# Optimization experiments

Hardware: AMD Instinct MI355X
Metric: run time of the kernel (lower is better)

Reference implementation:

```python
import jax, jax.numpy as jnp
import numpy as np

N_NODES = 50000
N_EDGES = 800000
D_IN = 128
D_OUT = 128
BN_EPS = 1e-5


def setup_inputs() -> dict:
    key = jax.random.key(0)
    ks = jax.random.split(key, 6)
    feat = jax.random.normal(ks[0], (N_NODES, D_IN), dtype=jnp.float32)
    src = jax.random.randint(ks[1], (N_EDGES,), 0, N_NODES, dtype=jnp.int32)
    dst = jax.random.randint(ks[2], (N_EDGES,), 0, N_NODES, dtype=jnp.int32)
    W = jax.random.normal(ks[3], (D_IN, D_OUT), dtype=jnp.float32) * (1.0 / np.sqrt(D_IN))
    b = jnp.zeros((D_OUT,), dtype=jnp.float32)
    a1 = jnp.full((1,), 0.25, dtype=jnp.float32)  # PReLU inside GraphConv
    gamma = jnp.ones((D_OUT,), dtype=jnp.float32)
    beta = jnp.zeros((D_OUT,), dtype=jnp.float32)
    a2 = jnp.full((1,), 0.25, dtype=jnp.float32)  # PReLU after BN
    return {"feat": feat, "src": src, "dst": dst, "W": W, "b": b,
            "a1": a1, "gamma": gamma, "beta": beta, "a2": a2}


def _prelu(x, a):
    return jnp.where(x >= 0, x, a * x)


def reference(feat, src, dst, W, b, a1, gamma, beta, a2):
    # Degrees (DGL clamps to min 1 to avoid inf norms)
    ones_e = jnp.ones((src.shape[0],), dtype=feat.dtype)
    out_deg = jnp.clip(jax.ops.segment_sum(ones_e, src, num_segments=N_NODES), 1.0)
    in_deg = jnp.clip(jax.ops.segment_sum(ones_e, dst, num_segments=N_NODES), 1.0)
    norm_src = jax.lax.rsqrt(out_deg)[:, None]   # [N,1]
    norm_dst = jax.lax.rsqrt(in_deg)[:, None]    # [N,1]

    # Dropout (eval mode -> identity), source normalization, projection
    h = (feat * norm_src) @ W                    # [N, D_OUT]
    # Gather-scatter neighbor aggregation (SpMM): sum over incoming edges
    msg = h[src]                                 # [E, D_OUT]
    agg = jax.ops.segment_sum(msg, dst, num_segments=N_NODES)  # [N, D_OUT]
    h = agg * norm_dst + b                       # dst normalization + bias
    h = _prelu(h, a1)                            # GraphConv activation

    # BatchNorm1d over node dimension (training-mode batch stats, biased var)
    mean = jnp.mean(h, axis=0)
    var = jnp.mean((h - mean) ** 2, axis=0)
    h = (h - mean) * jax.lax.rsqrt(var + BN_EPS) * gamma + beta

    return _prelu(h, a2)
```

## Files before the change

kernel.cpp:

```cpp
#include <hip/hip_runtime.h>
#include <hip/hip_bf16.h>

#define N_NODES 50000
#define N_EDGES 800000
#define D 128
#define BN_EPS 1e-5f
#define ELLW 64
#define PROJ_LDK 136
#define SPMM_BLOCKS 1564

#define BINS 128
#define BIN_RANGE 391
#define BINCAP 8192
#define A_EPT 13
#define A_BLOCKS 256

typedef __attribute__((ext_vector_type(8))) short bf16x8;
typedef __attribute__((ext_vector_type(4))) float f32x4;

__device__ inline float bf_lo(unsigned u) { union { unsigned x; float f; } c; c.x = u << 16; return c.f; }
__device__ inline float bf_hi(unsigned u) { union { unsigned x; float f; } c; c.x = u & 0xffff0000u; return c.f; }
__device__ inline unsigned short f2bf(float f) {
    union { float f; unsigned u; } c; c.f = f;
    unsigned u = c.u;
    u += 0x7fff + ((u >> 16) & 1);
    return (unsigned short)(u >> 16);
}
__device__ inline unsigned pack2bf(float a, float b) {
    return (unsigned)f2bf(a) | ((unsigned)f2bf(b) << 16);
}

__global__ __launch_bounds__(256) void bucket_kernel(const int* __restrict__ src,
                                                     const int* __restrict__ dst,
                                                     int* __restrict__ gdbase,
                                                     int* __restrict__ gsbase,
                                                     unsigned* __restrict__ dbkt,
                                                     unsigned short* __restrict__ sbkt) {
    __shared__ int dcnt[BINS], scnt[BINS], dbase[BINS], sbase[BINS];
    const int tid = threadIdx.x;
    if (tid < BINS) { dcnt[tid] = 0; scnt[tid] = 0; }
    __syncthreads();

    const int e0 = blockIdx.x * (256 * A_EPT) + tid;
    int s[A_EPT], t[A_EPT], dr[A_EPT], sr[A_EPT];
    #pragma unroll
    for (int k = 0; k < A_EPT; ++k) {
        int e = e0 + k * 256;
        if (e < N_EDGES) { s[k] = src[e]; t[k] = dst[e]; }
        else             { s[k] = -1;     t[k] = -1;     }
    }
    #pragma unroll
    for (int k = 0; k < A_EPT; ++k) {
        if (t[k] >= 0) dr[k] = atomicAdd(&dcnt[t[k] / BIN_RANGE], 1);
        if (s[k] >= 0) sr[k] = atomicAdd(&scnt[s[k] / BIN_RANGE], 1);
    }
    __syncthreads();
    if (tid < BINS) {
        dbase[tid] = atomicAdd(&gdbase[tid], dcnt[tid]);
        sbase[tid] = atomicAdd(&gsbase[tid], scnt[tid]);
    }
    __syncthreads();
    #pragma unroll
    for (int k = 0; k < A_EPT; ++k) {
        if (t[k] >= 0) {
            int b = t[k] / BIN_RANGE;
            int p = dbase[b] + dr[k];
            if (p < BINCAP)
                dbkt[b * BINCAP + p] = (unsigned)s[k] | ((unsigned)(t[k] - b * BIN_RANGE) << 16);
        }
        if (s[k] >= 0) {
            int b = s[k] / BIN_RANGE;
            int p = sbase[b] + sr[k];
            if (p < BINCAP)
                sbkt[b * BINCAP + p] = (unsigned short)(s[k] - b * BIN_RANGE);
        }
    }
}

__global__ __launch_bounds__(1024) void build_kernel(const int* __restrict__ gdbase,
                                                     const int* __restrict__ gsbase,
                                                     const unsigned* __restrict__ dbkt,
                                                     const unsigned short* __restrict__ sbkt,
                                                     unsigned short* __restrict__ ell,
                                                     int* __restrict__ cnt,
                                                     int* __restrict__ deg_out) {
    __shared__ int hist[BIN_RANGE];
    const int tid = threadIdx.x;
    const int bin = blockIdx.x & (BINS - 1);
    const int lo  = bin * BIN_RANGE;

    for (int i = tid; i < BIN_RANGE; i += 1024) hist[i] = 0;
    __syncthreads();

    if (blockIdx.x < BINS) {
        int count = gdbase[bin]; if (count > BINCAP) count = BINCAP;
        const unsigned* bkt = dbkt + bin * BINCAP;
        int i = tid;
        for (; i + 3072 < count; i += 4096) {
            unsigned e0 = bkt[i], e1 = bkt[i + 1024], e2 = bkt[i + 2048], e3 = bkt[i + 3072];
            int r0 = atomicAdd(&hist[e0 >> 16], 1);
            int r1 = atomicAdd(&hist[e1 >> 16], 1);
            int r2 = atomicAdd(&hist[e2 >> 16], 1);
            int r3 = atomicAdd(&hist[e3 >> 16], 1);
            if (r0 < ELLW) ell[(size_t)(lo + (e0 >> 16)) * ELLW + r0] = (unsigned short)(e0 & 0xffffu);
            if (r1 < ELLW) ell[(size_t)(lo + (e1 >> 16)) * ELLW + r1] = (unsigned short)(e1 & 0xffffu);
            if (r2 < ELLW) ell[(size_t)(lo + (e2 >> 16)) * ELLW + r2] = (unsigned short)(e2 & 0xffffu);
            if (r3 < ELLW) ell[(size_t)(lo + (e3 >> 16)) * ELLW + r3] = (unsigned short)(e3 & 0xffffu);
        }
        for (; i < count; i += 1024) {
            unsigned e = bkt[i];
            int r = atomicAdd(&hist[e >> 16], 1);
            if (r < ELLW) ell[(size_t)(lo + (e >> 16)) * ELLW + r] = (unsigned short)(e & 0xffffu);
        }
        __syncthreads();
        for (int j = tid; j < BIN_RANGE; j += 1024)
            if (lo + j < N_NODES) cnt[lo + j] = hist[j];
    } else {
        int count = gsbase[bin]; if (count > BINCAP) count = BINCAP;
        const unsigned short* bkt = sbkt + bin * BINCAP;
        int i = tid;
        for (; i + 3072 < count; i += 4096) {
            int v0 = bkt[i], v1 = bkt[i + 1024], v2 = bkt[i + 2048], v3 = bkt[i + 3072];
            atomicAdd(&hist[v0], 1); atomicAdd(&hist[v1], 1);
            atomicAdd(&hist[v2], 1); atomicAdd(&hist[v3], 1);
        }
        for (; i < count; i += 1024) atomicAdd(&hist[bkt[i]], 1);
        __syncthreads();
        for (int j = tid; j < BIN_RANGE; j += 1024)
            if (lo + j < N_NODES) deg_out[lo + j] = hist[j];
    }
}

__global__ __launch_bounds__(256, 2) void proj_kernel(const float* __restrict__ feat,
                                                      const float* __restrict__ W,
                                                      const int* __restrict__ deg_out,
                                                      unsigned short* __restrict__ h) {
    __shared__ unsigned short Wt[D * PROJ_LDK];
    __shared__ unsigned short As[64 * PROJ_LDK];
    __shared__ float nrmS[64];

    const int tid  = threadIdx.x;
    const int wave = tid >> 6;
    const int lane = tid & 63;
    const int quad = lane >> 4;
    const int l16  = lane & 15;

    for (int idx = tid; idx < D * D; idx += 256) {
        int k = idx >> 7, d = idx & 127;
        Wt[d * PROJ_LDK + k] = f2bf(W[idx]);
    }
    __syncthreads();

    bf16x8 breg[8][4];
    #pragma unroll
    for (int dt = 0; dt < 8; ++dt)
        #pragma unroll
        for (int kk = 0; kk < 4; ++kk)
            breg[dt][kk] = *(const bf16x8*)&Wt[(dt * 16 + l16) * PROJ_LDK + kk * 32 + quad * 8];

    const int n_tiles = (N_NODES + 63) / 64;
    for (int tile = blockIdx.x; tile < n_tiles; tile += gridDim.x) {
        const int base = tile * 64;
        __syncthreads();
        if (tid < 64) {
            int n = base + tid;
            int dg = (n < N_NODES) ? deg_out[n] : 1;
            nrmS[tid] = rsqrtf((float)(dg < 1 ? 1 : dg));
        }
        __syncthreads();
        for (int idx = tid; idx < 64 * 32; idx += 256) {
            int r = idx >> 5, c4 = idx & 31;
            int n = base + r;
            float4 v = (n < N_NODES) ? ((const float4*)(feat + (size_t)n * D))[c4]
                                     : make_float4(0.f, 0.f, 0.f, 0.f);
            float nm = nrmS[r];
            unsigned short* pp = &As[r * PROJ_LDK + c4 * 4];
            pp[0] = f2bf(v.x * nm); pp[1] = f2bf(v.y * nm);
            pp[2] = f2bf(v.z * nm); pp[3] = f2bf(v.w * nm);
        }
        __syncthreads();

        f32x4 acc[8];
        #pragma unroll
        for (int dt = 0; dt < 8; ++dt) acc[dt] = (f32x4){0.f, 0.f, 0.f, 0.f};

        #pragma unroll
        for (int kk = 0; kk < 4; ++kk) {
            bf16x8 af = *(const bf16x8*)&As[(wave * 16 + l16) * PROJ_LDK + kk * 32 + quad * 8];
            #pragma unroll
            for (int dt = 0; dt < 8; ++dt)
                acc[dt] = __builtin_amdgcn_mfma_f32_16x16x32_bf16(af, breg[dt][kk], acc[dt], 0, 0, 0);
        }

        #pragma unroll
        for (int dt = 0; dt < 8; ++dt) {
            #pragma unroll
            for (int r = 0; r < 4; ++r) {
                int n = base + wave * 16 + quad * 4 + r;
                if (n < N_NODES)
                    h[(size_t)n * D + dt * 16 + l16] = f2bf(acc[dt][r]);
            }
        }
    }
}

#define ACCA(v) { accA[0] += bf_lo((v).x); accA[1] += bf_hi((v).x); \
                  accA[2] += bf_lo((v).y); accA[3] += bf_hi((v).y); \
                  accA[4] += bf_lo((v).z); accA[5] += bf_hi((v).z); \
                  accA[6] += bf_lo((v).w); accA[7] += bf_hi((v).w); }
#define ACCB(v) { accB[0] += bf_lo((v).x); accB[1] += bf_hi((v).x); \
                  accB[2] += bf_lo((v).y); accB[3] += bf_hi((v).y); \
                  accB[4] += bf_lo((v).z); accB[5] += bf_hi((v).z); \
                  accB[6] += bf_lo((v).w); accB[7] += bf_hi((v).w); }
#define GA(sid) { uint4 vv = *(const uint4*)(h + (size_t)(sid) * D + coff); ACCA(vv); }
#define GB(sid) { uint4 vv = *(const uint4*)(h + (size_t)(sid) * D + coff); ACCB(vv); }

__global__ __launch_bounds__(256) void spmm_kernel(const int* __restrict__ cnt,
                                                   const unsigned short* __restrict__ ell,
                                                   const unsigned short* __restrict__ h,
                                                   const float* __restrict__ b,
                                                   const float* __restrict__ a1,
                                                   unsigned short* __restrict__ h2,
                                                   float* __restrict__ bn_sum,
                                                   float* __restrict__ bn_sumsq) {
    const int tid  = threadIdx.x;
    const int l16  = tid & 15;
    const int slot = (blockIdx.x * 256 + tid) >> 4;
    const float alpha = a1[0];
    const size_t coff = (size_t)l16 * 8;

    float bias[8];
    #pragma unroll
    for (int j = 0; j < 8; ++j) bias[j] = b[l16 * 8 + j];

    float lsum[8] = {0,0,0,0,0,0,0,0};
    float lsq[8]  = {0,0,0,0,0,0,0,0};

    if (slot < N_NODES / 2) {
        const int n0 = slot * 2;
        const int n1 = n0 + 1;
        int dgA = cnt[n0], dgB = cnt[n1];
        int endA = (dgA < ELLW) ? dgA : ELLW;
        int endB = (dgB < ELLW) ? dgB : ELLW;
        const unsigned short* rowA = ell + (size_t)n0 * ELLW;
        const unsigned short* rowB = ell + (size_t)n1 * ELLW;

        float accA[8] = {0,0,0,0,0,0,0,0};
        float accB[8] = {0,0,0,0,0,0,0,0};
        int iA = 0, iB = 0;

        while (iA + 8 <= endA && iB + 8 <= endB) {
            uint4 ra = *(const uint4*)(rowA + iA);
            uint4 rb = *(const uint4*)(rowB + iB);
            GA(ra.x & 0xffff); GA(ra.x >> 16);
            GA(ra.y & 0xffff); GA(ra.y >> 16);
            GA(ra.z & 0xffff); GA(ra.z >> 16);
            GA(ra.w & 0xffff); GA(ra.w >> 16);
            GB(rb.x & 0xffff); GB(rb.x >> 16);
            GB(rb.y & 0xffff); GB(rb.y >> 16);
            GB(rb.z & 0xffff); GB(rb.z >> 16);
            GB(rb.w & 0xffff); GB(rb.w >> 16);
            iA += 8; iB += 8;
        }
        for (; iA + 8 <= endA; iA += 8) {
            uint4 ra = *(const uint4*)(rowA + iA);
            GA(ra.x & 0xffff); GA(ra.x >> 16);
            GA(ra.y & 0xffff); GA(ra.y >> 16);
            GA(ra.z & 0xffff); GA(ra.z >> 16);
            GA(ra.w & 0xffff); GA(ra.w >> 16);
        }
        for (; iB + 8 <= endB; iB += 8) {
            uint4 rb = *(const uint4*)(rowB + iB);
            GB(rb.x & 0xffff); GB(rb.x >> 16);
            GB(rb.y & 0xffff); GB(rb.y >> 16);
            GB(rb.z & 0xffff); GB(rb.z >> 16);
            GB(rb.w & 0xffff); GB(rb.w >> 16);
        }
        for (; iA < endA; ++iA) { GA(rowA[iA]); }
        for (; iB < endB; ++iB) { GB(rowB[iB]); }

        float ndA = rsqrtf((float)(dgA < 1 ? 1 : dgA));
        float ndB = rsqrtf((float)(dgB < 1 ? 1 : dgB));
        float xA[8], xB[8];
        #pragma unroll
        for (int j = 0; j < 8; ++j) {
            float va = accA[j] * ndA + bias[j];
            va = (va >= 0.f) ? va : alpha * va;
            xA[j] = va; lsum[j] += va; lsq[j] += va * va;
            float vb = accB[j] * ndB + bias[j];
            vb = (vb >= 0.f) ? vb : alpha * vb;
            xB[j] = vb; lsum[j] += vb; lsq[j] += vb * vb;
        }
        uint4 oA, oB;
        oA.x = pack2bf(xA[0], xA[1]); oA.y = pack2bf(xA[2], xA[3]);
        oA.z = pack2bf(xA[4], xA[5]); oA.w = pack2bf(xA[6], xA[7]);
        oB.x = pack2bf(xB[0], xB[1]); oB.y = pack2bf(xB[2], xB[3]);
        oB.z = pack2bf(xB[4], xB[5]); oB.w = pack2bf(xB[6], xB[7]);
        *(uint4*)(h2 + (size_t)n0 * D + coff) = oA;
        *(uint4*)(h2 + (size_t)n1 * D + coff) = oB;
    }

    #pragma unroll
    for (int j = 0; j < 8; ++j) {
        lsum[j] += __shfl_xor(lsum[j], 16);
        lsum[j] += __shfl_xor(lsum[j], 32);
        lsq[j]  += __shfl_xor(lsq[j], 16);
        lsq[j]  += __shfl_xor(lsq[j], 32);
    }
    __shared__ float red[4][256];
    const int wave = tid >> 6;
    const int lane = tid & 63;
    if (lane < 16) {
        #pragma unroll
        for (int j = 0; j < 8; ++j) {
            red[wave][l16 * 16 + j]     = lsum[j];
            red[wave][l16 * 16 + 8 + j] = lsq[j];
        }
    }
    __syncthreads();
    {
        float tot = red[0][tid] + red[1][tid] + red[2][tid] + red[3][tid];
        int l = tid >> 4;
        int v = tid & 15;
        int dim = l * 8 + (v & 7);
        int rep = (blockIdx.x & 3) * D;
        if (v < 8) atomicAdd(&bn_sum[rep + dim], tot);
        else       atomicAdd(&bn_sumsq[rep + dim], tot);
    }
}

__global__ __launch_bounds__(256) void final_kernel(const unsigned short* __restrict__ h2,
                                                    const float* __restrict__ bn_sum,
                                                    const float* __restrict__ bn_sumsq,
                                                    const float* __restrict__ gamma,
                                                    const float* __restrict__ beta,
                                                    const float* __restrict__ a2,
                                                    float* __restrict__ out) {
    int i8 = blockIdx.x * 256 + threadIdx.x;
    if (i8 < N_NODES * D / 8) {
        int dbase = (i8 * 8) & (D - 1);
        const float invN = 1.0f / (float)N_NODES;
        const float alpha = a2[0];
        uint4 v = ((const uint4*)h2)[i8];
        float xv[8] = { bf_lo(v.x), bf_hi(v.x), bf_lo(v.y), bf_hi(v.y),
                        bf_lo(v.z), bf_hi(v.z), bf_lo(v.w), bf_hi(v.w) };
        float r[8];
        #pragma unroll
        for (int j = 0; j < 8; ++j) {
            int d = dbase + j;
            float sm = bn_sum[d] + bn_sum[D + d] + bn_sum[2 * D + d] + bn_sum[3 * D + d];
            float sq = bn_sumsq[d] + bn_sumsq[D + d] + bn_sumsq[2 * D + d] + bn_sumsq[3 * D + d];
            float mean = sm * invN;
            float var  = sq * invN - mean * mean;
            float inv  = rsqrtf(var + BN_EPS);
            float t = (xv[j] - mean) * inv * gamma[d] + beta[d];
            r[j] = (t >= 0.f) ? t : alpha * t;
        }
        float4* po = (float4*)(out + (size_t)i8 * 8);
        po[0] = make_float4(r[0], r[1], r[2], r[3]);
        po[1] = make_float4(r[4], r[5], r[6], r[7]);
    }
}

extern "C" void kernel_launch(void* const* d_in, const int* in_sizes, int n_in,
                              void* d_out, int out_size, void* d_ws, size_t ws_size,
                              hipStream_t stream) {
    const float* feat  = (const float*)d_in[0];
    const int*   src   = (const int*)  d_in[1];
    const int*   dst   = (const int*)  d_in[2];
    const float* W     = (const float*)d_in[3];
    const float* b     = (const float*)d_in[4];
    const float* a1    = (const float*)d_in[5];
    const float* gamma = (const float*)d_in[6];
    const float* beta  = (const float*)d_in[7];
    const float* a2    = (const float*)d_in[8];
    float* out = (float*)d_out;

    char* ws = (char*)d_ws;
    int*            gdbase    = (int*)(ws + 0);
    int*            gsbase    = (int*)(ws + 512);
    float*          bn_sum    = (float*)(ws + 1024);
    float*          bn_sumsq  = (float*)(ws + 3072);
    int*            cnt       = (int*)(ws + 5120);
    int*            deg_out_p = (int*)(ws + 205120);
    unsigned short* ell       = (unsigned short*)(ws + 405120);
    unsigned short* h         = (unsigned short*)(ws + 6805120);
    unsigned short* h2        = (unsigned short*)(ws + 19605120);
    unsigned*       dbkt      = (unsigned*)(ws + 32405120);
    unsigned short* sbkt      = (unsigned short*)(ws + 36599424);

    hipMemsetAsync(ws, 0, 5120, stream);

    bucket_kernel<<<A_BLOCKS, 256, 0, stream>>>(src, dst, gdbase, gsbase, dbkt, sbkt);

    build_kernel<<<2 * BINS, 1024, 0, stream>>>(gdbase, gsbase, dbkt, sbkt,
                                                ell, cnt, deg_out_p);

    proj_kernel<<<391, 256, 0, stream>>>(feat, W, deg_out_p, h);

    spmm_kernel<<<SPMM_BLOCKS, 256, 0, stream>>>(cnt, ell, h, b, a1, h2, bn_sum, bn_sumsq);

    final_kernel<<<(N_NODES * D / 8 + 255) / 256, 256, 0, stream>>>(h2, bn_sum, bn_sumsq,
                                                                    gamma, beta, a2, out);
}
```

Measured before the change: 183.1 us.

## Fuse SpMM and BatchNorm finalize via cooperative grid sync; drop proj LDS staging

SpMM aggregation and the BatchNorm/PReLU finalize now run in one cooperative kernel. Each thread keeps its four node rows in registers across a grid-wide sync, so the bf16 intermediate h2 is never written to or re-read from global memory. The projection kernel now loads feat rows straight into MFMA A-fragments instead of staging them through LDS with extra barriers, and it launches more blocks. The cost is a grid sync and lower per-block occupancy flexibility; if the cooperative launch fails, the code falls back to the original two kernels.

```diff
diff --git a/kernel.cpp b/kernel.cpp
--- a/kernel.cpp
+++ b/kernel.cpp
@@ -1,5 +1,8 @@
 #include <hip/hip_runtime.h>
 #include <hip/hip_bf16.h>
+#include <hip/hip_cooperative_groups.h>
+
+namespace cg = cooperative_groups;
 
 #define N_NODES 50000
 #define N_EDGES 800000
@@ -8,6 +11,7 @@
 #define ELLW 64
 #define PROJ_LDK 136
 #define SPMM_BLOCKS 1564
+#define FUSED_BLOCKS 782
 
 #define BINS 128
 #define BIN_RANGE 391
@@ -136,8 +140,6 @@
                                                       const int* __restrict__ deg_out,
                                                       unsigned short* __restrict__ h) {
     __shared__ unsigned short Wt[D * PROJ_LDK];
-    __shared__ unsigned short As[64 * PROJ_LDK];
-    __shared__ float nrmS[64];
 
     const int tid  = threadIdx.x;
     const int wave = tid >> 6;
@@ -161,24 +163,13 @@
     const int n_tiles = (N_NODES + 63) / 64;
     for (int tile = blockIdx.x; tile < n_tiles; tile += gridDim.x) {
         const int base = tile * 64;
-        __syncthreads();
-        if (tid < 64) {
-            int n = base + tid;
-            int dg = (n < N_NODES) ? deg_out[n] : 1;
-            nrmS[tid] = rsqrtf((float)(dg < 1 ? 1 : dg));
-        }
-        __syncthreads();
-        for (int idx = tid; idx < 64 * 32; idx += 256) {
-            int r = idx >> 5, c4 = idx & 31;
-            int n = base + r;
-            float4 v = (n < N_NODES) ? ((const float4*)(feat + (size_t)n * D))[c4]
-                                     : make_float4(0.f, 0.f, 0.f, 0.f);
-            float nm = nrmS[r];
-            unsigned short* pp = &As[r * PROJ_LDK + c4 * 4];
-            pp[0] = f2bf(v.x * nm); pp[1] = f2bf(v.y * nm);
-            pp[2] = f2bf(v.z * nm); pp[3] = f2bf(v.w * nm);
-        }
-        __syncthreads();
+        const int arow = base + wave * 16 + l16;
+        const bool rok = arow < N_NODES;
+        float nm;
+        {
+            int dg = rok ? deg_out[arow] : 1;
+            nm = rsqrtf((float)(dg < 1 ? 1 : dg));
+        }
 
         f32x4 acc[8];
         #pragma unroll
@@ -186,7 +177,17 @@
 
         #pragma unroll
         for (int kk = 0; kk < 4; ++kk) {
-            bf16x8 af = *(const bf16x8*)&As[(wave * 16 + l16) * PROJ_LDK + kk * 32 + quad * 8];
+            bf16x8 af;
+            if (rok) {
+                const float4* fp = (const float4*)(feat + (size_t)arow * D + kk * 32 + quad * 8);
+                float4 f0 = fp[0], f1 = fp[1];
+                af[0] = (short)f2bf(f0.x * nm); af[1] = (short)f2bf(f0.y * nm);
+                af[2] = (short)f2bf(f0.z * nm); af[3] = (short)f2bf(f0.w * nm);
+                af[4] = (short)f2bf(f1.x * nm); af[5] = (short)f2bf(f1.y * nm);
+                af[6] = (short)f2bf(f1.z * nm); af[7] = (short)f2bf(f1.w * nm);
+            } else {
+                af = (bf16x8){0, 0, 0, 0, 0, 0, 0, 0};
+            }
             #pragma unroll
             for (int dt = 0; dt < 8; ++dt)
                 acc[dt] = __builtin_amdgcn_mfma_f32_16x16x32_bf16(af, breg[dt][kk], acc[dt], 0, 0, 0);
@@ -214,6 +215,160 @@
                   accB[6] += bf_lo((v).w); accB[7] += bf_hi((v).w); }
 #define GA(sid) { uint4 vv = *(const uint4*)(h + (size_t)(sid) * D + coff); ACCA(vv); }
 #define GB(sid) { uint4 vv = *(const uint4*)(h + (size_t)(sid) * D + coff); ACCB(vv); }
+
+__device__ __forceinline__ void gather_pair(int n0, int n1,
+                                            const int* __restrict__ cnt,
+                                            const unsigned short* __restrict__ ell,
+                                            const unsigned short* __restrict__ h,
+                                            size_t coff, const float* bias, float alpha,
+                                            float (&xA)[8], float (&xB)[8],
+                                            float (&lsum)[8], float (&lsq)[8]) {
+    int dgA = cnt[n0], dgB = cnt[n1];
+    int endA = (dgA < ELLW) ? dgA : ELLW;
+    int endB = (dgB < ELLW) ? dgB : ELLW;
+    const unsigned short* rowA = ell + (size_t)n0 * ELLW;
+    const unsigned short* rowB = ell + (size_t)n1 * ELLW;
+
+    float accA[8] = {0,0,0,0,0,0,0,0};
+    float accB[8] = {0,0,0,0,0,0,0,0};
+    int iA = 0, iB = 0;
+
+    while (iA + 8 <= endA && iB + 8 <= endB) {
+        uint4 ra = *(const uint4*)(rowA + iA);
+        uint4 rb = *(const uint4*)(rowB + iB);
+        GA(ra.x & 0xffff); GA(ra.x >> 16);
+        GA(ra.y & 0xffff); GA(ra.y >> 16);
+        GA(ra.z & 0xffff); GA(ra.z >> 16);
+        GA(ra.w & 0xffff); GA(ra.w >> 16);
+        GB(rb.x & 0xffff); GB(rb.x >> 16);
+        GB(rb.y & 0xffff); GB(rb.y >> 16);
+        GB(rb.z & 0xffff); GB(rb.z >> 16);
+        GB(rb.w & 0xffff); GB(rb.w >> 16);
+        iA += 8; iB += 8;
+    }
+    for (; iA + 8 <= endA; iA += 8) {
+        uint4 ra = *(const uint4*)(rowA + iA);
+        GA(ra.x & 0xffff); GA(ra.x >> 16);
+        GA(ra.y & 0xffff); GA(ra.y >> 16);
+        GA(ra.z & 0xffff); GA(ra.z >> 16);
+        GA(ra.w & 0xffff); GA(ra.w >> 16);
+    }
+    for (; iB + 8 <= endB; iB += 8) {
+        uint4 rb = *(const uint4*)(rowB + iB);
+        GB(rb.x & 0xffff); GB(rb.x >> 16);
+        GB(rb.y & 0xffff); GB(rb.y >> 16);
+        GB(rb.z & 0xffff); GB(rb.z >> 16);
+        GB(rb.w & 0xffff); GB(rb.w >> 16);
+    }
+    for (; iA < endA; ++iA) { GA(rowA[iA]); }
+    for (; iB < endB; ++iB) { GB(rowB[iB]); }
+
+    float ndA = rsqrtf((float)(dgA < 1 ? 1 : dgA));
+    float ndB = rsqrtf((float)(dgB < 1 ? 1 : dgB));
+    #pragma unroll
+    for (int j = 0; j < 8; ++j) {
+        float va = accA[j] * ndA + bias[j];
+        va = (va >= 0.f) ? va : alpha * va;
+        xA[j] = va; lsum[j] += va; lsq[j] += va * va;
+        float vb = accB[j] * ndB + bias[j];
+        vb = (vb >= 0.f) ? vb : alpha * vb;
+        xB[j] = vb; lsum[j] += vb; lsq[j] += vb * vb;
+    }
+}
+
+__global__ __launch_bounds__(256, 4) void spmm_final_kernel(
+        const int* __restrict__ cnt,
+        const unsigned short* __restrict__ ell,
+        const unsigned short* __restrict__ h,
+        const float* __restrict__ b,
+        const float* __restrict__ a1,
+        const float* __restrict__ gamma,
+        const float* __restrict__ beta,
+        const float* __restrict__ a2,
+        float* __restrict__ out,
+        float* __restrict__ bn_sum,
+        float* __restrict__ bn_sumsq) {
+    const int tid  = threadIdx.x;
+    const int l16  = tid & 15;
+    const int slot = (blockIdx.x * 256 + tid) >> 4;
+    const float alpha = a1[0];
+    const size_t coff = (size_t)l16 * 8;
+
+    float bias[8];
+    #pragma unroll
+    for (int j = 0; j < 8; ++j) bias[j] = b[l16 * 8 + j];
+
+    float lsum[8] = {0,0,0,0,0,0,0,0};
+    float lsq[8]  = {0,0,0,0,0,0,0,0};
+    float x0[8], x1[8], x2[8], x3[8];
+
+    const bool active = (slot < N_NODES / 4);
+    const int nb = slot * 4;
+    if (active) {
+        gather_pair(nb,     nb + 1, cnt, ell, h, coff, bias, alpha, x0, x1, lsum, lsq);
+        gather_pair(nb + 2, nb + 3, cnt, ell, h, coff, bias, alpha, x2, x3, lsum, lsq);
+    }
+
+    #pragma unroll
+    for (int j = 0; j < 8; ++j) {
+        lsum[j] += __shfl_xor(lsum[j], 16);
+        lsum[j] += __shfl_xor(lsum[j], 32);
+        lsq[j]  += __shfl_xor(lsq[j], 16);
+        lsq[j]  += __shfl_xor(lsq[j], 32);
+    }
+    __shared__ float red[4][256];
+    const int wave = tid >> 6;
+    const int lane = tid & 63;
+    if (lane < 16) {
+        #pragma unroll
+        for (int j = 0; j < 8; ++j) {
+            red[wave][l16 * 16 + j]     = lsum[j];
+            red[wave][l16 * 16 + 8 + j] = lsq[j];
+        }
+    }
+    __syncthreads();
+    {
+        float tot = red[0][tid] + red[1][tid] + red[2][tid] + red[3][tid];
+        int l = tid >> 4;
+        int v = tid & 15;
+        int dim = l * 8 + (v & 7);
+        int rep = (blockIdx.x & 3) * D;
+        if (v < 8) atomicAdd(&bn_sum[rep + dim], tot);
+        else       atomicAdd(&bn_sumsq[rep + dim], tot);
+    }
+    __threadfence();
+    cg::this_grid().sync();
+
+    if (active) {
+        const float invN = 1.0f / (float)N_NODES;
+        const float alpha2 = a2[0];
+        float r0[8], r1[8], r2[8], r3[8];
+        #pragma unroll
+        for (int j = 0; j < 8; ++j) {
+            int d = l16 * 8 + j;
+            float sm = bn_sum[d] + bn_sum[D + d] + bn_sum[2 * D + d] + bn_sum[3 * D + d];
+            float sq = bn_sumsq[d] + bn_sumsq[D + d] + bn_sumsq[2 * D + d] + bn_sumsq[3 * D + d];
+            float mean = sm * invN;
+            float var  = sq * invN - mean * mean;
+            float inv  = rsqrtf(var + BN_EPS);
+            float gs = inv * gamma[d];
+            float bt = beta[d] - mean * gs;
+            float t;
+            t = x0[j] * gs + bt; r0[j] = (t >= 0.f) ? t : alpha2 * t;
+            t = x1[j] * gs + bt; r1[j] = (t >= 0.f) ? t : alpha2 * t;
+            t = x2[j] * gs + bt; r2[j] = (t >= 0.f) ? t : alpha2 * t;
+            t = x3[j] * gs + bt; r3[j] = (t >= 0.f) ? t : alpha2 * t;
+        }
+        float4* p0 = (float4*)(out + (size_t)nb * D + coff);
+        float4* p1 = (float4*)(out + (size_t)(nb + 1) * D + coff);
+        float4* p2 = (float4*)(out + (size_t)(nb + 2) * D + coff);
+        float4* p3 = (float4*)(out + (size_t)(nb + 3) * D + coff);
+        p0[0] = make_float4(r0[0], r0[1], r0[2], r0[3]); p0[1] = make_float4(r0[4], r0[5], r0[6], r0[7]);
+        p1[0] = make_float4(r1[0], r1[1], r1[2], r1[3]); p1[1] = make_float4(r1[4], r1[5], r1[6], r1[7]);
+        p2[0] = make_float4(r2[0], r2[1], r2[2], r2[3]); p2[1] = make_float4(r2[4], r2[5], r2[6], r2[7]);
+        p3[0] = make_float4(r3[0], r3[1], r3[2], r3[3]); p3[1] = make_float4(r3[4], r3[5], r3[6], r3[7]);
+    }
+}
 
 __global__ __launch_bounds__(256) void spmm_kernel(const int* __restrict__ cnt,
                                                    const unsigned short* __restrict__ ell,
@@ -239,58 +394,8 @@
     if (slot < N_NODES / 2) {
         const int n0 = slot * 2;
         const int n1 = n0 + 1;
-        int dgA = cnt[n0], dgB = cnt[n1];
-        int endA = (dgA < ELLW) ? dgA : ELLW;
-        int endB = (dgB < ELLW) ? dgB : ELLW;
-        const unsigned short* rowA = ell + (size_t)n0 * ELLW;
-        const unsigned short* rowB = ell + (size_t)n1 * ELLW;
-
-        float accA[8] = {0,0,0,0,0,0,0,0};
-        float accB[8] = {0,0,0,0,0,0,0,0};
-        int iA = 0, iB = 0;
-
-        while (iA + 8 <= endA && iB + 8 <= endB) {
-            uint4 ra = *(const uint4*)(rowA + iA);
-            uint4 rb = *(const uint4*)(rowB + iB);
-            GA(ra.x & 0xffff); GA(ra.x >> 16);
-            GA(ra.y & 0xffff); GA(ra.y >> 16);
-            GA(ra.z & 0xffff); GA(ra.z >> 16);
-            GA(ra.w & 0xffff); GA(ra.w >> 16);
-            GB(rb.x & 0xffff); GB(rb.x >> 16);
-            GB(rb.y & 0xffff); GB(rb.y >> 16);
-            GB(rb.z & 0xffff); GB(rb.z >> 16);
-            GB(rb.w & 0xffff); GB(rb.w >> 16);
-            iA += 8; iB += 8;
-        }
-        for (; iA + 8 <= endA; iA += 8) {
-            uint4 ra = *(const uint4*)(rowA + iA);
-            GA(ra.x & 0xffff); GA(ra.x >> 16);
-            GA(ra.y & 0xffff); GA(ra.y >> 16);
-            GA(ra.z & 0xffff); GA(ra.z >> 16);
-            GA(ra.w & 0xffff); GA(ra.w >> 16);
-        }
-        for (; iB + 8 <= endB; iB += 8) {
-            uint4 rb = *(const uint4*)(rowB + iB);
-            GB(rb.x & 0xffff); GB(rb.x >> 16);
-            GB(rb.y & 0xffff); GB(rb.y >> 16);
-            GB(rb.z & 0xffff); GB(rb.z >> 16);
-            GB(rb.w & 0xffff); GB(rb.w >> 16);
-        }
-        for (; iA < endA; ++iA) { GA(rowA[iA]); }
-        for (; iB < endB; ++iB) { GB(rowB[iB]); }
-
-        float ndA = rsqrtf((float)(dgA < 1 ? 1 : dgA));
-        float ndB = rsqrtf((float)(dgB < 1 ? 1 : dgB));
         float xA[8], xB[8];
-        #pragma unroll
-        for (int j = 0; j < 8; ++j) {
-            float va = accA[j] * ndA + bias[j];
-            va = (va >= 0.f) ? va : alpha * va;
-            xA[j] = va; lsum[j] += va; lsq[j] += va * va;
-            float vb = accB[j] * ndB + bias[j];
-            vb = (vb >= 0.f) ? vb : alpha * vb;
-            xB[j] = vb; lsum[j] += vb; lsq[j] += vb * vb;
-        }
+        gather_pair(n0, n1, cnt, ell, h, coff, bias, alpha, xA, xB, lsum, lsq);
         uint4 oA, oB;
         oA.x = pack2bf(xA[0], xA[1]); oA.y = pack2bf(xA[2], xA[3]);
         oA.z = pack2bf(xA[4], xA[5]); oA.w = pack2bf(xA[6], xA[7]);
@@ -396,10 +501,23 @@
     build_kernel<<<2 * BINS, 1024, 0, stream>>>(gdbase, gsbase, dbkt, sbkt,
                                                 ell, cnt, deg_out_p);
 
-    proj_kernel<<<391, 256, 0, stream>>>(feat, W, deg_out_p, h);
-
-    spmm_kernel<<<SPMM_BLOCKS, 256, 0, stream>>>(cnt, ell, h, b, a1, h2, bn_sum, bn_sumsq);
-
-    final_kernel<<<(N_NODES * D / 8 + 255) / 256, 256, 0, stream>>>(h2, bn_sum, bn_sumsq,
-                                                                    gamma, beta, a2, out);
-}
+    proj_kernel<<<FUSED_BLOCKS, 256, 0, stream>>>(feat, W, deg_out_p, h);
+
+    {
+        const int*            cnt_a   = cnt;
+        const unsigned short* ell_a   = ell;
+        const unsigned short* h_a     = h;
+        void* args[] = { (void*)&cnt_a, (void*)&ell_a, (void*)&h_a,
+                         (void*)&b, (void*)&a1, (void*)&gamma, (void*)&beta,
+                         (void*)&a2, (void*)&out, (void*)&bn_sum, (void*)&bn_sumsq };
+        hipError_t err = hipLaunchCooperativeKernel((const void*)spmm_final_kernel,
+                                                    dim3(FUSED_BLOCKS), dim3(256),
+                                                    args, 0, stream);
+        if (err != hipSuccess) {
+            spmm_kernel<<<SPMM_BLOCKS, 256, 0, stream>>>(cnt, ell, h, b, a1, h2,
+                                                         bn_sum, bn_sumsq);
+            final_kernel<<<(N_NODES * D / 8 + 255) / 256, 256, 0, stream>>>(
+                h2, bn_sum, bn_sumsq, gamma, beta, a2, out);
+        }
+    }
+}
```

After: 339.7 us. 1.86x slower.
